# Kernel optimization log

Hardware: AMD Instinct MI355X
Metric: run time of the kernel (lower is better)

## Reference

```python
import jax, jax.numpy as jnp
import numpy as np

B, T, H = 4, 4096, 1024


def setup_inputs() -> dict:
    key = jax.random.key(0)
    k1, k2 = jax.random.split(key)
    h = jax.random.normal(k1, (B, T, H), dtype=jnp.float32)
    # nn.Linear weight, scaled for stable magnitudes
    W = jax.random.normal(k2, (H, H), dtype=jnp.float32) / np.sqrt(H).astype(np.float32)
    return {"h": h, "W": W, "T_hist": 256}


def reference(h, W, T_hist):
    Bb, Tt, Hh = h.shape
    # K = Linear(h) = h @ W.T ; Q = V = h
    K = jnp.einsum('bth,oh->bto', h, W)
    scores = jnp.einsum('bqh,bkh->bqk', h, K) / jnp.sqrt(jnp.asarray(Hh, h.dtype))
    # banded mask: causal (j <= i) AND limited history (j >= i - (T_hist-1))
    i = jnp.arange(Tt)[:, None]
    j = jnp.arange(Tt)[None, :]
    valid = (j <= i) & (j >= i - (T_hist - 1))
    scores = jnp.where(valid[None, :, :], scores, -jnp.inf)
    attn = jax.nn.softmax(scores, axis=-1)
    attn = jnp.nan_to_num(attn, nan=0.0)  # matches torch nan_to_num(0.0)
    context = jnp.einsum('bqk,bkh->bqh', attn, h)
    return context
```

## Files before the change

### kernel.cpp

```cpp
#include <hip/hip_runtime.h>
#include <hip/hip_bf16.h>

#define B_ 4
#define T_ 4096
#define H_ 1024
#define WP2 320

typedef short  s16x8 __attribute__((ext_vector_type(8)));
typedef float  f32x4 __attribute__((ext_vector_type(4)));
typedef unsigned short u16;

static __device__ __forceinline__ u16 bf16rn(float f) {
  unsigned int u = __float_as_uint(f);
  u += 0x7fffu + ((u >> 16) & 1u);
  return (u16)(u >> 16);
}

static __device__ __forceinline__ void gl2lds16(const u16* g, u16* l) {
  __builtin_amdgcn_global_load_lds(
      (__attribute__((address_space(1))) void*)(g),
      (__attribute__((address_space(3))) void*)(l), 16, 0, 0);
}

__global__ __launch_bounds__(256) void k_convT(const float* __restrict__ h,
                                               u16* __restrict__ hb,
                                               u16* __restrict__ hbT) {
  __shared__ unsigned int tile32[64 * 33];
  const int b  = blockIdx.z;
  const int t0 = blockIdx.y * 64;
  const int c0 = blockIdx.x * 64;
  const int t  = threadIdx.x;
  {
    const int r  = t >> 2;
    const int cq = (t & 3) << 4;
    const size_t g = (size_t)(b * T_ + t0 + r) * H_ + c0 + cq;
    const f32x4* src = (const f32x4*)(h + g);
    u16 o[16];
#pragma unroll
    for (int v = 0; v < 4; ++v) {
      f32x4 x = src[v];
#pragma unroll
      for (int j = 0; j < 4; ++j) o[v * 4 + j] = bf16rn(x[j]);
    }
    s16x8 w0, w1;
#pragma unroll
    for (int j = 0; j < 8; ++j) { w0[j] = (short)o[j]; w1[j] = (short)o[8 + j]; }
    *(s16x8*)(hb + g)     = w0;
    *(s16x8*)(hb + g + 8) = w1;
#pragma unroll
    for (int i = 0; i < 8; ++i)
      tile32[r * 33 + (cq >> 1) + i] =
          (unsigned int)o[2 * i] | ((unsigned int)o[2 * i + 1] << 16);
  }
  __syncthreads();
  {
    const int fpair = t & 31;
    const int kq    = t >> 5;
    unsigned int v[8];
#pragma unroll
    for (int j = 0; j < 8; ++j) v[j] = tile32[(kq * 8 + j) * 33 + fpair];
    s16x8 w0, w1;
#pragma unroll
    for (int j = 0; j < 8; ++j) {
      w0[j] = (short)(v[j] & 0xffffu);
      w1[j] = (short)(v[j] >> 16);
    }
    const size_t o0 = (size_t)(b * H_ + c0 + 2 * fpair) * T_ + t0 + kq * 8;
    *(s16x8*)(hbT + o0)      = w0;
    *(s16x8*)(hbT + o0 + T_) = w1;
  }
}

__global__ __launch_bounds__(256) void k_convW(const float* __restrict__ src,
                                               u16* __restrict__ dst) {
  const int i = (blockIdx.x * 256 + threadIdx.x) * 8;
  f32x4 a = *(const f32x4*)(src + i);
  f32x4 b = *(const f32x4*)(src + i + 4);
  s16x8 w;
#pragma unroll
  for (int j = 0; j < 4; ++j) {
    w[j]     = (short)bf16rn(a[j]);
    w[4 + j] = (short)bf16rn(b[j]);
  }
  *(s16x8*)(dst + i) = w;
}

__global__ __launch_bounds__(256) void k_gemmK(const u16* __restrict__ hb,
                                               const u16* __restrict__ Wb,
                                               u16* __restrict__ Kb) {
  __shared__ __align__(16) u16 As[1024 * 8];
  __shared__ __align__(16) u16 Bs[1024 * 8];
  const int t = threadIdx.x;
  const int id  = blockIdx.y * gridDim.x + blockIdx.x;
  const int swz = (id & 7) * 128 + (id >> 3);
  const int row0 = (swz >> 3) * 128;
  const int col0 = (swz & 7) * 128;
  const int lane = t & 63, wv = t >> 6;
  const int wr = wv >> 1, wc = wv & 1;
  const int l15 = lane & 15, quad = lane >> 4;

  int cc[4];
  size_t gA[4], gB[4];
#pragma unroll
  for (int p = 0; p < 4; ++p) {
    const int c = p * 256 + t;
    cc[p] = c;
    const int ks = c >> 9, row = (c >> 2) & 127, qd = c & 3;
    const int colo = ks * 32 + qd * 8;
    gA[p] = (size_t)(row0 + row) * H_ + colo;
    gB[p] = (size_t)(col0 + row) * H_ + colo;
  }

  f32x4 acc[4][4];
#pragma unroll
  for (int m = 0; m < 4; ++m)
#pragma unroll
    for (int n = 0; n < 4; ++n) acc[m][n] = (f32x4)0.0f;

  for (int k0 = 0; k0 < H_; k0 += 64) {
    __syncthreads();
#pragma unroll
    for (int p = 0; p < 4; ++p) {
      gl2lds16(hb + gA[p] + k0, &As[cc[p] * 8]);
      gl2lds16(Wb + gB[p] + k0, &Bs[cc[p] * 8]);
    }
    __syncthreads();
#pragma unroll
    for (int ks = 0; ks < 2; ++ks) {
      s16x8 aF[4], bF[4];
#pragma unroll
      for (int mt = 0; mt < 4; ++mt)
        aF[mt] = *(const s16x8*)
            &As[(ks * 512 + (wr * 64 + mt * 16 + l15) * 4 + quad) * 8];
#pragma unroll
      for (int nt = 0; nt < 4; ++nt)
        bF[nt] = *(const s16x8*)
            &Bs[(ks * 512 + (wc * 64 + nt * 16 + l15) * 4 + quad) * 8];
#pragma unroll
      for (int mt = 0; mt < 4; ++mt)
#pragma unroll
        for (int nt = 0; nt < 4; ++nt)
          acc[mt][nt] = __builtin_amdgcn_mfma_f32_16x16x32_bf16(
              aF[mt], bF[nt], acc[mt][nt], 0, 0, 0);
    }
  }
#pragma unroll
  for (int mt = 0; mt < 4; ++mt)
#pragma unroll
    for (int nt = 0; nt < 4; ++nt)
#pragma unroll
      for (int r = 0; r < 4; ++r) {
        const int row = row0 + wr * 64 + mt * 16 + quad * 4 + r;
        const int col = col0 + wc * 64 + nt * 16 + l15;
        Kb[(size_t)row * H_ + col] = bf16rn(acc[mt][nt][r]);
      }
}

__global__ __launch_bounds__(512) void k_scores(const u16* __restrict__ hb,
                                                const u16* __restrict__ Kb,
                                                u16* __restrict__ P) {
  __shared__ __align__(16) u16 Ks[2][1152 * 8];
  __shared__ float Sred[2][4][16];
  const int t = threadIdx.x;
  const int wv = t >> 6, lane = t & 63;
  const int l15 = lane & 15, quad = lane >> 4;
  const int id  = blockIdx.x;
  const int swz = (id & 7) * 64 + (id >> 3);
  const int b  = swz >> 7;
  const int q0 = (swz & 127) * 32;
  const int qt = wv & 1;
  const int sub = wv >> 1;
  const int qt0 = q0 + qt * 16;
  const int ktbase = (sub == 0) ? 0 : (1 + sub * 4);
  const int nkt = (sub == 0) ? 5 : 4;

  const u16* qbase = hb + (size_t)(b * T_ + qt0 + l15) * H_ + quad * 8;

  const u16* kst[3];
  int cid[3];
#pragma unroll
  for (int p = 0; p < 3; ++p) {
    int c = p * 512 + t;
    if (c > 1151) c = 1151;
    cid[p] = c;
    const int m = c >> 6, lr = (c >> 2) & 15, qd = c & 3;
    int tok = q0 - 256 + m * 16 + lr;
    if (tok < 0) tok = 0;
    kst[p] = Kb + (size_t)(b * T_ + tok) * H_ + qd * 8;
  }
  const bool p2 = (t < 128);

  f32x4 acc[5];
#pragma unroll
  for (int i = 0; i < 5; ++i) acc[i] = (f32x4)0.0f;

  gl2lds16(kst[0], &Ks[0][cid[0] * 8]);
  gl2lds16(kst[1], &Ks[0][cid[1] * 8]);
  if (p2) gl2lds16(kst[2], &Ks[0][cid[2] * 8]);
  __syncthreads();

  int cur = 0;
  for (int s = 0; s < 32; ++s) {
    if (s + 1 < 32) {
      const int off = (s + 1) * 32;
      gl2lds16(kst[0] + off, &Ks[cur ^ 1][cid[0] * 8]);
      gl2lds16(kst[1] + off, &Ks[cur ^ 1][cid[1] * 8]);
      if (p2) gl2lds16(kst[2] + off, &Ks[cur ^ 1][cid[2] * 8]);
    }
    const s16x8 aQ = *(const s16x8*)(qbase + s * 32);
#pragma unroll
    for (int i = 0; i < 5; ++i) {
      if (i < nkt) {
        const int m = qt + ktbase + i;
        const s16x8 bK = *(const s16x8*)&Ks[cur][(m * 64 + l15 * 4 + quad) * 8];
        acc[i] = __builtin_amdgcn_mfma_f32_16x16x32_bf16(aQ, bK, acc[i], 0, 0, 0);
      }
    }
    __syncthreads();
    cur ^= 1;
  }

  const float scale = 0.03125f;
#pragma unroll
  for (int r = 0; r < 4; ++r) {
    const int q = qt0 + quad * 4 + r;
    float sum = 0.0f;
#pragma unroll
    for (int i = 0; i < 5; ++i) {
      if (i < nkt) {
        const int k = qt0 - 256 + (ktbase + i) * 16 + l15;
        const bool valid = (k >= 0) && (k <= q) && (k >= q - 255);
        const float p = valid ? __expf(acc[i][r] * scale) : 0.0f;
        acc[i][r] = p;
        sum += p;
      }
    }
    sum += __shfl_xor(sum, 1);
    sum += __shfl_xor(sum, 2);
    sum += __shfl_xor(sum, 4);
    sum += __shfl_xor(sum, 8);
    if (l15 == 0) Sred[qt][sub][quad * 4 + r] = sum;
  }
  __syncthreads();
  const int toff = ((q0 & 32) >> 4) + qt;
#pragma unroll
  for (int r = 0; r < 4; ++r) {
    const int q = qt0 + quad * 4 + r;
    const int row = quad * 4 + r;
    const float inv = 1.0f / (Sred[qt][0][row] + Sred[qt][1][row] +
                              Sred[qt][2][row] + Sred[qt][3][row]);
    u16* prow = P + (size_t)(b * T_ + q) * WP2;
#pragma unroll
    for (int i = 0; i < 5; ++i)
      if (i < nkt) prow[(toff + ktbase + i) * 16 + l15] = bf16rn(acc[i][r] * inv);
    if (sub == 0) {
#pragma unroll
      for (int z = 0; z < 3; ++z) {
        const int slot = (toff + 17 + z) % 20;
        prow[slot * 16 + l15] = 0;
      }
    }
  }
}

__global__ __launch_bounds__(512) void k_ctx(const u16* __restrict__ P,
                                             const u16* __restrict__ hbT,
                                             float* __restrict__ out) {
  __shared__ __align__(16) u16 Vs[2][1280 * 8];
  const int t = threadIdx.x;
  const int wv = t >> 6, lane = t & 63;
  const int l15 = lane & 15, quad = lane >> 4;
  const int id  = blockIdx.x;
  const int swz = (id & 7) * 64 + (id >> 3);
  const int fhalf = swz & 1;
  const int blk   = swz >> 1;
  const int b  = blk >> 6;
  const int q0 = (blk & 63) * 64;
  const int qtile = wv & 3, fh = wv >> 2;
  const int qt0 = q0 + qtile * 16;

  const u16* prow = P + (size_t)(b * T_ + qt0 + l15) * WP2 + quad * 8;
  s16x8 aP[10];
#pragma unroll
  for (int c = 0; c < 10; ++c) aP[c] = *(const s16x8*)(prow + c * 32);

  const int tok0 = q0 - 256;
  const u16* vst[3];
  int cid[3];
#pragma unroll
  for (int p = 0; p < 3; ++p) {
    int c = p * 512 + t;
    if (c > 1279) c = 1279;
    cid[p] = c;
    const int cg = c >> 7, ft = (c >> 6) & 1, lr = (c >> 2) & 15, qd = c & 3;
    const int fr = ft * 16 + lr;
    int tok = tok0 + (cg * 4 + qd) * 8;
    if (tok < 0) tok = 0;
    vst[p] = hbT + (size_t)(b * H_ + fr) * T_ + tok;
  }
  const bool p2 = (t < 256);
  const size_t fbase = (size_t)(fhalf * 512) * T_;
  const size_t fstep = (size_t)32 * T_;

  gl2lds16(vst[0] + fbase, &Vs[0][cid[0] * 8]);
  gl2lds16(vst[1] + fbase, &Vs[0][cid[1] * 8]);
  if (p2) gl2lds16(vst[2] + fbase, &Vs[0][cid[2] * 8]);
  __syncthreads();

  int cur = 0;
  for (int g = 0; g < 16; ++g) {
    if (g + 1 < 16) {
      const size_t off = fbase + (size_t)(g + 1) * fstep;
      gl2lds16(vst[0] + off, &Vs[cur ^ 1][cid[0] * 8]);
      gl2lds16(vst[1] + off, &Vs[cur ^ 1][cid[1] * 8]);
      if (p2) gl2lds16(vst[2] + off, &Vs[cur ^ 1][cid[2] * 8]);
    }
    f32x4 acc = (f32x4)0.0f;
#pragma unroll
    for (int c = 0; c < 10; ++c) {
      const s16x8 bv =
          *(const s16x8*)&Vs[cur][(c * 128 + fh * 64 + l15 * 4 + quad) * 8];
      acc = __builtin_amdgcn_mfma_f32_16x16x32_bf16(aP[c], bv, acc, 0, 0, 0);
    }
    __syncthreads();
    const int f0 = (fhalf * 16 + g) * 32 + fh * 16 + l15;
#pragma unroll
    for (int r = 0; r < 4; ++r)
      out[(size_t)(b * T_ + qt0 + quad * 4 + r) * H_ + f0] = acc[r];
    cur ^= 1;
  }
}

extern "C" void kernel_launch(void* const* d_in, const int* in_sizes, int n_in,
                              void* d_out, int out_size, void* d_ws, size_t ws_size,
                              hipStream_t stream) {
  const float* h  = (const float*)d_in[0];
  const float* Wf = (const float*)d_in[1];

  char* ws = (char*)d_ws;
  u16* hb  = (u16*)(ws);
  u16* hbT = (u16*)(ws + (size_t)33554432);
  u16* Kb  = (u16*)(ws + (size_t)67108864);
  u16* Wb  = (u16*)(ws + (size_t)100663296);
  u16* P   = (u16*)(ws + (size_t)102760448);
  float* out = (float*)d_out;

  k_convT <<<dim3(H_ / 64, T_ / 64, B_), 256, 0, stream>>>(h, hb, hbT);
  k_convW <<<dim3(512), 256, 0, stream>>>(Wf, Wb);
  k_gemmK <<<dim3(H_ / 128, (B_ * T_) / 128), 256, 0, stream>>>(hb, Wb, Kb);
  k_scores<<<dim3((B_ * T_) / 32), 512, 0, stream>>>(hb, Kb, P);
  k_ctx   <<<dim3(2 * (B_ * T_) / 64), 512, 0, stream>>>(P, hbT, out);
}
```

Measured before the change: 233.0 us.

## Double-buffer K-projection GEMM and widen score tiles to 64 queries per block

The K-projection GEMM now steps through K in chunks of 32 with double-buffered LDS, prefetching the next chunk while MFMAs run on the current one. This replaces two barriers per iteration with one and lets loads overlap compute. The scores kernel now handles 64 query rows per 256-thread block, and every wave computes all 20 key tiles of the shared band window. That halves the K data loaded per query row and removes the cross-wave softmax-sum reduction through shared memory. The cost is extra MFMA work on tiles that are fully masked, plus more accumulator registers per wave.

```diff
diff --git a/kernel.cpp b/kernel.cpp
--- a/kernel.cpp
+++ b/kernel.cpp
@@ -88,8 +88,8 @@
 __global__ __launch_bounds__(256) void k_gemmK(const u16* __restrict__ hb,
                                                const u16* __restrict__ Wb,
                                                u16* __restrict__ Kb) {
-  __shared__ __align__(16) u16 As[1024 * 8];
-  __shared__ __align__(16) u16 Bs[1024 * 8];
+  __shared__ __align__(16) u16 As[2][512 * 8];
+  __shared__ __align__(16) u16 Bs[2][512 * 8];
   const int t = threadIdx.x;
   const int id  = blockIdx.y * gridDim.x + blockIdx.x;
   const int swz = (id & 7) * 128 + (id >> 3);
@@ -99,17 +99,11 @@
   const int wr = wv >> 1, wc = wv & 1;
   const int l15 = lane & 15, quad = lane >> 4;
 
-  int cc[4];
-  size_t gA[4], gB[4];
-#pragma unroll
-  for (int p = 0; p < 4; ++p) {
-    const int c = p * 256 + t;
-    cc[p] = c;
-    const int ks = c >> 9, row = (c >> 2) & 127, qd = c & 3;
-    const int colo = ks * 32 + qd * 8;
-    gA[p] = (size_t)(row0 + row) * H_ + colo;
-    gB[p] = (size_t)(col0 + row) * H_ + colo;
-  }
+  const int c0 = t, c1 = t + 256;
+  const size_t gA0 = (size_t)(row0 + (c0 >> 2)) * H_ + (c0 & 3) * 8;
+  const size_t gA1 = (size_t)(row0 + (c1 >> 2)) * H_ + (c1 & 3) * 8;
+  const size_t gB0 = (size_t)(col0 + (c0 >> 2)) * H_ + (c0 & 3) * 8;
+  const size_t gB1 = (size_t)(col0 + (c1 >> 2)) * H_ + (c1 & 3) * 8;
 
   f32x4 acc[4][4];
 #pragma unroll
@@ -117,32 +111,36 @@
 #pragma unroll
     for (int n = 0; n < 4; ++n) acc[m][n] = (f32x4)0.0f;
 
-  for (int k0 = 0; k0 < H_; k0 += 64) {
+  gl2lds16(hb + gA0, &As[0][c0 * 8]);
+  gl2lds16(hb + gA1, &As[0][c1 * 8]);
+  gl2lds16(Wb + gB0, &Bs[0][c0 * 8]);
+  gl2lds16(Wb + gB1, &Bs[0][c1 * 8]);
+  __syncthreads();
+
+  int cur = 0;
+  for (int kt = 0; kt < 32; ++kt) {
+    if (kt + 1 < 32) {
+      const int off = (kt + 1) * 32;
+      gl2lds16(hb + gA0 + off, &As[cur ^ 1][c0 * 8]);
+      gl2lds16(hb + gA1 + off, &As[cur ^ 1][c1 * 8]);
+      gl2lds16(Wb + gB0 + off, &Bs[cur ^ 1][c0 * 8]);
+      gl2lds16(Wb + gB1 + off, &Bs[cur ^ 1][c1 * 8]);
+    }
+    s16x8 aF[4], bF[4];
+#pragma unroll
+    for (int mt = 0; mt < 4; ++mt)
+      aF[mt] = *(const s16x8*)&As[cur][((wr * 64 + mt * 16 + l15) * 4 + quad) * 8];
+#pragma unroll
+    for (int nt = 0; nt < 4; ++nt)
+      bF[nt] = *(const s16x8*)&Bs[cur][((wc * 64 + nt * 16 + l15) * 4 + quad) * 8];
+#pragma unroll
+    for (int mt = 0; mt < 4; ++mt)
+#pragma unroll
+      for (int nt = 0; nt < 4; ++nt)
+        acc[mt][nt] = __builtin_amdgcn_mfma_f32_16x16x32_bf16(aF[mt], bF[nt],
+                                                              acc[mt][nt], 0, 0, 0);
     __syncthreads();
-#pragma unroll
-    for (int p = 0; p < 4; ++p) {
-      gl2lds16(hb + gA[p] + k0, &As[cc[p] * 8]);
-      gl2lds16(Wb + gB[p] + k0, &Bs[cc[p] * 8]);
-    }
-    __syncthreads();
-#pragma unroll
-    for (int ks = 0; ks < 2; ++ks) {
-      s16x8 aF[4], bF[4];
-#pragma unroll
-      for (int mt = 0; mt < 4; ++mt)
-        aF[mt] = *(const s16x8*)
-            &As[(ks * 512 + (wr * 64 + mt * 16 + l15) * 4 + quad) * 8];
-#pragma unroll
-      for (int nt = 0; nt < 4; ++nt)
-        bF[nt] = *(const s16x8*)
-            &Bs[(ks * 512 + (wc * 64 + nt * 16 + l15) * 4 + quad) * 8];
-#pragma unroll
-      for (int mt = 0; mt < 4; ++mt)
-#pragma unroll
-        for (int nt = 0; nt < 4; ++nt)
-          acc[mt][nt] = __builtin_amdgcn_mfma_f32_16x16x32_bf16(
-              aF[mt], bF[nt], acc[mt][nt], 0, 0, 0);
-    }
+    cur ^= 1;
   }
 #pragma unroll
   for (int mt = 0; mt < 4; ++mt)
@@ -156,65 +154,53 @@
       }
 }
 
-__global__ __launch_bounds__(512) void k_scores(const u16* __restrict__ hb,
-                                                const u16* __restrict__ Kb,
-                                                u16* __restrict__ P) {
-  __shared__ __align__(16) u16 Ks[2][1152 * 8];
-  __shared__ float Sred[2][4][16];
+__global__ __launch_bounds__(256, 2) void k_scores(const u16* __restrict__ hb,
+                                                   const u16* __restrict__ Kb,
+                                                   u16* __restrict__ P) {
+  __shared__ __align__(16) u16 Ks[2][1280 * 8];
   const int t = threadIdx.x;
   const int wv = t >> 6, lane = t & 63;
   const int l15 = lane & 15, quad = lane >> 4;
   const int id  = blockIdx.x;
-  const int swz = (id & 7) * 64 + (id >> 3);
-  const int b  = swz >> 7;
-  const int q0 = (swz & 127) * 32;
-  const int qt = wv & 1;
-  const int sub = wv >> 1;
-  const int qt0 = q0 + qt * 16;
-  const int ktbase = (sub == 0) ? 0 : (1 + sub * 4);
-  const int nkt = (sub == 0) ? 5 : 4;
+  const int swz = (id & 7) * 32 + (id >> 3);
+  const int b  = swz >> 6;
+  const int q0 = (swz & 63) * 64;
+  const int qt0 = q0 + wv * 16;
+  const int tok0 = q0 - 256;
 
   const u16* qbase = hb + (size_t)(b * T_ + qt0 + l15) * H_ + quad * 8;
 
-  const u16* kst[3];
-  int cid[3];
-#pragma unroll
-  for (int p = 0; p < 3; ++p) {
-    int c = p * 512 + t;
-    if (c > 1151) c = 1151;
-    cid[p] = c;
+  const u16* kst[5];
+#pragma unroll
+  for (int p = 0; p < 5; ++p) {
+    const int c = p * 256 + t;
     const int m = c >> 6, lr = (c >> 2) & 15, qd = c & 3;
-    int tok = q0 - 256 + m * 16 + lr;
+    int tok = tok0 + m * 16 + lr;
     if (tok < 0) tok = 0;
     kst[p] = Kb + (size_t)(b * T_ + tok) * H_ + qd * 8;
   }
-  const bool p2 = (t < 128);
-
-  f32x4 acc[5];
-#pragma unroll
-  for (int i = 0; i < 5; ++i) acc[i] = (f32x4)0.0f;
-
-  gl2lds16(kst[0], &Ks[0][cid[0] * 8]);
-  gl2lds16(kst[1], &Ks[0][cid[1] * 8]);
-  if (p2) gl2lds16(kst[2], &Ks[0][cid[2] * 8]);
+
+  f32x4 acc[20];
+#pragma unroll
+  for (int j = 0; j < 20; ++j) acc[j] = (f32x4)0.0f;
+
+#pragma unroll
+  for (int p = 0; p < 5; ++p) gl2lds16(kst[p], &Ks[0][(p * 256 + t) * 8]);
   __syncthreads();
 
   int cur = 0;
   for (int s = 0; s < 32; ++s) {
     if (s + 1 < 32) {
       const int off = (s + 1) * 32;
-      gl2lds16(kst[0] + off, &Ks[cur ^ 1][cid[0] * 8]);
-      gl2lds16(kst[1] + off, &Ks[cur ^ 1][cid[1] * 8]);
-      if (p2) gl2lds16(kst[2] + off, &Ks[cur ^ 1][cid[2] * 8]);
+#pragma unroll
+      for (int p = 0; p < 5; ++p)
+        gl2lds16(kst[p] + off, &Ks[cur ^ 1][(p * 256 + t) * 8]);
     }
     const s16x8 aQ = *(const s16x8*)(qbase + s * 32);
 #pragma unroll
-    for (int i = 0; i < 5; ++i) {
-      if (i < nkt) {
-        const int m = qt + ktbase + i;
-        const s16x8 bK = *(const s16x8*)&Ks[cur][(m * 64 + l15 * 4 + quad) * 8];
-        acc[i] = __builtin_amdgcn_mfma_f32_16x16x32_bf16(aQ, bK, acc[i], 0, 0, 0);
-      }
+    for (int j = 0; j < 20; ++j) {
+      const s16x8 bK = *(const s16x8*)&Ks[cur][(j * 64 + l15 * 4 + quad) * 8];
+      acc[j] = __builtin_amdgcn_mfma_f32_16x16x32_bf16(aQ, bK, acc[j], 0, 0, 0);
     }
     __syncthreads();
     cur ^= 1;
@@ -226,40 +212,22 @@
     const int q = qt0 + quad * 4 + r;
     float sum = 0.0f;
 #pragma unroll
-    for (int i = 0; i < 5; ++i) {
-      if (i < nkt) {
-        const int k = qt0 - 256 + (ktbase + i) * 16 + l15;
-        const bool valid = (k >= 0) && (k <= q) && (k >= q - 255);
-        const float p = valid ? __expf(acc[i][r] * scale) : 0.0f;
-        acc[i][r] = p;
-        sum += p;
-      }
+    for (int j = 0; j < 20; ++j) {
+      const int k = tok0 + j * 16 + l15;
+      const bool valid = (k >= 0) && (k <= q) && (k >= q - 255);
+      const float p = valid ? __expf(acc[j][r] * scale) : 0.0f;
+      acc[j][r] = p;
+      sum += p;
     }
     sum += __shfl_xor(sum, 1);
     sum += __shfl_xor(sum, 2);
     sum += __shfl_xor(sum, 4);
     sum += __shfl_xor(sum, 8);
-    if (l15 == 0) Sred[qt][sub][quad * 4 + r] = sum;
-  }
-  __syncthreads();
-  const int toff = ((q0 & 32) >> 4) + qt;
-#pragma unroll
-  for (int r = 0; r < 4; ++r) {
-    const int q = qt0 + quad * 4 + r;
-    const int row = quad * 4 + r;
-    const float inv = 1.0f / (Sred[qt][0][row] + Sred[qt][1][row] +
-                              Sred[qt][2][row] + Sred[qt][3][row]);
+    const float inv = 1.0f / sum;
     u16* prow = P + (size_t)(b * T_ + q) * WP2;
 #pragma unroll
-    for (int i = 0; i < 5; ++i)
-      if (i < nkt) prow[(toff + ktbase + i) * 16 + l15] = bf16rn(acc[i][r] * inv);
-    if (sub == 0) {
-#pragma unroll
-      for (int z = 0; z < 3; ++z) {
-        const int slot = (toff + 17 + z) % 20;
-        prow[slot * 16 + l15] = 0;
-      }
-    }
+    for (int j = 0; j < 20; ++j)
+      prow[j * 16 + l15] = bf16rn(acc[j][r] * inv);
   }
 }
 
@@ -348,6 +316,6 @@
   k_convT <<<dim3(H_ / 64, T_ / 64, B_), 256, 0, stream>>>(h, hb, hbT);
   k_convW <<<dim3(512), 256, 0, stream>>>(Wf, Wb);
   k_gemmK <<<dim3(H_ / 128, (B_ * T_) / 128), 256, 0, stream>>>(hb, Wb, Kb);
-  k_scores<<<dim3((B_ * T_) / 32), 512, 0, stream>>>(hb, Kb, P);
+  k_scores<<<dim3((B_ * T_) / 64), 256, 0, stream>>>(hb, Kb, P);
   k_ctx   <<<dim3(2 * (B_ * T_) / 64), 512, 0, stream>>>(P, hbT, out);
 }
```

After: 232.6 us. Within noise of the previous version (-0.2%).

## Triple-buffer K-projection GEMM loads with async global-to-LDS prefetch

Applied to the files above, without the earlier changes.

Restructures the K = h·Wᵀ GEMM main loop from a load-then-compute loop with two barriers per 64-wide k step into a three-stage ring of 32-wide k slices. Loads for slice kt+2 are issued before the MFMAs on slice kt, gated by vmcnt waits and one barrier per step. The aim is to hide global memory latency behind tensor-core work and cut barrier count. The risks are a fully unrolled 32-iteration loop that raises code size and register pressure, and correctness that depends on hand-placed waitcnt values.

```diff
diff --git a/kernel.cpp b/kernel.cpp
--- a/kernel.cpp
+++ b/kernel.cpp
@@ -88,8 +88,8 @@
 __global__ __launch_bounds__(256) void k_gemmK(const u16* __restrict__ hb,
                                                const u16* __restrict__ Wb,
                                                u16* __restrict__ Kb) {
-  __shared__ __align__(16) u16 As[1024 * 8];
-  __shared__ __align__(16) u16 Bs[1024 * 8];
+  __shared__ __align__(16) u16 As[3][512 * 8];
+  __shared__ __align__(16) u16 Bs[3][512 * 8];
   const int t = threadIdx.x;
   const int id  = blockIdx.y * gridDim.x + blockIdx.x;
   const int swz = (id & 7) * 128 + (id >> 3);
@@ -99,17 +99,11 @@
   const int wr = wv >> 1, wc = wv & 1;
   const int l15 = lane & 15, quad = lane >> 4;
 
-  int cc[4];
-  size_t gA[4], gB[4];
-#pragma unroll
-  for (int p = 0; p < 4; ++p) {
-    const int c = p * 256 + t;
-    cc[p] = c;
-    const int ks = c >> 9, row = (c >> 2) & 127, qd = c & 3;
-    const int colo = ks * 32 + qd * 8;
-    gA[p] = (size_t)(row0 + row) * H_ + colo;
-    gB[p] = (size_t)(col0 + row) * H_ + colo;
-  }
+  const int c0 = t, c1 = t + 256;
+  const size_t gA0 = (size_t)(row0 + (c0 >> 2)) * H_ + (c0 & 3) * 8;
+  const size_t gA1 = (size_t)(row0 + (c1 >> 2)) * H_ + (c1 & 3) * 8;
+  const size_t gB0 = (size_t)(col0 + (c0 >> 2)) * H_ + (c0 & 3) * 8;
+  const size_t gB1 = (size_t)(col0 + (c1 >> 2)) * H_ + (c1 & 3) * 8;
 
   f32x4 acc[4][4];
 #pragma unroll
@@ -117,31 +111,45 @@
 #pragma unroll
     for (int n = 0; n < 4; ++n) acc[m][n] = (f32x4)0.0f;
 
-  for (int k0 = 0; k0 < H_; k0 += 64) {
-    __syncthreads();
-#pragma unroll
-    for (int p = 0; p < 4; ++p) {
-      gl2lds16(hb + gA[p] + k0, &As[cc[p] * 8]);
-      gl2lds16(Wb + gB[p] + k0, &Bs[cc[p] * 8]);
-    }
-    __syncthreads();
-#pragma unroll
-    for (int ks = 0; ks < 2; ++ks) {
-      s16x8 aF[4], bF[4];
-#pragma unroll
-      for (int mt = 0; mt < 4; ++mt)
-        aF[mt] = *(const s16x8*)
-            &As[(ks * 512 + (wr * 64 + mt * 16 + l15) * 4 + quad) * 8];
+  gl2lds16(hb + gA0, &As[0][c0 * 8]);
+  gl2lds16(hb + gA1, &As[0][c1 * 8]);
+  gl2lds16(Wb + gB0, &Bs[0][c0 * 8]);
+  gl2lds16(Wb + gB1, &Bs[0][c1 * 8]);
+  gl2lds16(hb + gA0 + 32, &As[1][c0 * 8]);
+  gl2lds16(hb + gA1 + 32, &As[1][c1 * 8]);
+  gl2lds16(Wb + gB0 + 32, &Bs[1][c0 * 8]);
+  gl2lds16(Wb + gB1 + 32, &Bs[1][c1 * 8]);
+  asm volatile("s_waitcnt vmcnt(4)" ::: "memory");
+  __builtin_amdgcn_s_barrier();
+
+#pragma unroll
+  for (int kt = 0; kt < 32; ++kt) {
+    if (kt + 2 < 32) {
+      const int sn = (kt + 2) % 3;
+      const int off = (kt + 2) * 32;
+      gl2lds16(hb + gA0 + off, &As[sn][c0 * 8]);
+      gl2lds16(hb + gA1 + off, &As[sn][c1 * 8]);
+      gl2lds16(Wb + gB0 + off, &Bs[sn][c0 * 8]);
+      gl2lds16(Wb + gB1 + off, &Bs[sn][c1 * 8]);
+    }
+    const int sc = kt % 3;
+    s16x8 aF[4], bF[4];
+#pragma unroll
+    for (int mt = 0; mt < 4; ++mt)
+      aF[mt] = *(const s16x8*)&As[sc][((wr * 64 + mt * 16 + l15) * 4 + quad) * 8];
+#pragma unroll
+    for (int nt = 0; nt < 4; ++nt)
+      bF[nt] = *(const s16x8*)&Bs[sc][((wc * 64 + nt * 16 + l15) * 4 + quad) * 8];
+#pragma unroll
+    for (int mt = 0; mt < 4; ++mt)
 #pragma unroll
       for (int nt = 0; nt < 4; ++nt)
-        bF[nt] = *(const s16x8*)
-            &Bs[(ks * 512 + (wc * 64 + nt * 16 + l15) * 4 + quad) * 8];
-#pragma unroll
-      for (int mt = 0; mt < 4; ++mt)
-#pragma unroll
-        for (int nt = 0; nt < 4; ++nt)
-          acc[mt][nt] = __builtin_amdgcn_mfma_f32_16x16x32_bf16(
-              aF[mt], bF[nt], acc[mt][nt], 0, 0, 0);
+        acc[mt][nt] = __builtin_amdgcn_mfma_f32_16x16x32_bf16(aF[mt], bF[nt],
+                                                              acc[mt][nt], 0, 0, 0);
+    if (kt + 1 < 32) {
+      if (kt <= 29) asm volatile("s_waitcnt vmcnt(4)" ::: "memory");
+      else          asm volatile("s_waitcnt vmcnt(0)" ::: "memory");
+      __builtin_amdgcn_s_barrier();
     }
   }
 #pragma unroll
```

Measured after the change: 227.1 us. -2.5%, faster.
